# Performance work log

Hardware: AMD Instinct MI355X
Metric: run time of the kernel (lower is better)

## Reference

```python
import jax, jax.numpy as jnp
import numpy as np

B, N, F, C = 8, 4096, 1024, 64


def setup_inputs() -> dict:
    key = jax.random.key(0)
    k1, k2, k3 = jax.random.split(key, 3)
    x1 = jax.random.normal(k1, (B, N, F), dtype=jnp.float32)
    x2 = jax.random.normal(k2, (B, N, F), dtype=jnp.float32)
    W = jax.random.normal(k3, (C, F), dtype=jnp.float32) / np.sqrt(F)
    b = jnp.zeros((C,), dtype=jnp.float32)
    return {"x1": x1, "x2": x2, "W": W, "b": b}


def _select_max(x, W, b):
    # x: [B, N, F] -> scores [B, N, C]
    scores = jnp.einsum("bnf,cf->bnc", x, W) + b
    # per-batch, per-class index of max-scoring instance: [B, C]
    idx = jnp.argmax(scores, axis=1)
    # gather the selected instance feature vectors: [B, C, F]
    return jnp.take_along_axis(x, idx[:, :, None], axis=1)


def reference(x1, x2, W, b):
    d = _select_max(x1, W, b)
    d1 = _select_max(x2, W, b)
    return (d, d1)
```

## Files before the change

kernel.cpp:

```cpp
#include <hip/hip_runtime.h>

#define B_   8
#define N_   4096
#define F_   1024
#define C_   64
#define MARGIN 0.08f

typedef __attribute__((ext_vector_type(8))) short bhalf8;
typedef __attribute__((ext_vector_type(4))) float f32x4;

__device__ __forceinline__ unsigned short f2bf_rne(float x) {
    unsigned u = __builtin_bit_cast(unsigned, x);
    u += 0x7fffu + ((u >> 16) & 1u);
    return (unsigned short)(u >> 16);
}
__device__ __forceinline__ bhalf8 cvt8(float4 a, float4 b) {
    bhalf8 r;
    r[0] = (short)f2bf_rne(a.x); r[1] = (short)f2bf_rne(a.y);
    r[2] = (short)f2bf_rne(a.z); r[3] = (short)f2bf_rne(a.w);
    r[4] = (short)f2bf_rne(b.x); r[5] = (short)f2bf_rne(b.y);
    r[6] = (short)f2bf_rne(b.z); r[7] = (short)f2bf_rne(b.w);
    return r;
}

#define LEXGT(a, ai, b, bi) ((a) > (b) || ((a) == (b) && (ai) < (bi)))
#define INSERT3(vv, nn)                                                        \
    do {                                                                       \
        float _v = (vv); int _n = (nn);                                        \
        if (LEXGT(_v, _n, v0, i0)) { v2=v1; i2=i1; v1=v0; i1=i0; v0=_v; i0=_n; } \
        else if (LEXGT(_v, _n, v1, i1)) { v2=v1; i2=i1; v1=_v; i1=_n; }        \
        else if (LEXGT(_v, _n, v2, i2)) { v2=_v; i2=_n; }                      \
    } while (0)
#define INSERT4(vv, nn)                                                        \
    do {                                                                       \
        float _v = (vv); int _n = (nn);                                        \
        if (LEXGT(_v, _n, v0, i0)) { v3=v2; i3=i2; v2=v1; i2=i1; v1=v0; i1=i0; v0=_v; i0=_n; } \
        else if (LEXGT(_v, _n, v1, i1)) { v3=v2; i3=i2; v2=v1; i2=i1; v1=_v; i1=_n; } \
        else if (LEXGT(_v, _n, v2, i2)) { v3=v2; i3=i2; v2=_v; i2=_n; }        \
        else if (LEXGT(_v, _n, v3, i3)) { v3=_v; i3=_n; }                      \
    } while (0)

__global__ __launch_bounds__(512, 2) void score_top_kernel(
    const float* __restrict__ x1, const float* __restrict__ x2,
    const float* __restrict__ W,
    float* __restrict__ pv, int* __restrict__ pi)
{
    __shared__ __align__(16) char lds[131072];

    const int tid  = threadIdx.x;
    const int nb   = blockIdx.x;
    const int b    = blockIdx.y;
    const int inp  = blockIdx.z;
    const float* __restrict__ x = inp ? x2 : x1;

    const int lane = tid & 63;
    const int w    = tid >> 6;
    const int rsel = lane & 15;
    const int g    = lane >> 4;
    const int swz  = (rsel & 7) << 4;

    #pragma unroll
    for (int j = 0; j < 16; ++j) {
        int gi = tid + 512 * j;
        int c = gi >> 7, kq = gi & 127;
        const float* src = W + (size_t)c * F_ + kq * 8;
        float4 a  = *(const float4*)src;
        float4 bq = *(const float4*)(src + 4);
        int off = (c * 2048 + kq * 16) ^ ((c & 7) << 4);
        *(bhalf8*)(lds + off) = cvt8(a, bq);
    }

    const int row = nb * 128 + w * 16 + rsel;
    const float* __restrict__ xr = x + ((size_t)b * N_ + row) * F_ + g * 8;

    f32x4 acc[4];
    #pragma unroll
    for (int nt = 0; nt < 4; ++nt) acc[nt] = (f32x4){0.f, 0.f, 0.f, 0.f};

    auto loadx = [&](float4* dst, int kc) {
        #pragma unroll
        for (int st = 0; st < 2; ++st) {
            dst[2 * st]     = *(const float4*)(xr + kc * 64 + st * 32);
            dst[2 * st + 1] = *(const float4*)(xr + kc * 64 + st * 32 + 4);
        }
    };
    auto compute = [&](const float4* src, int kc) {
        #pragma unroll
        for (int st = 0; st < 2; ++st) {
            bhalf8 ah = cvt8(src[2 * st], src[2 * st + 1]);
            int kb = (kc * 64 + st * 32 + g * 8) * 2;
            #pragma unroll
            for (int nt = 0; nt < 4; ++nt) {
                int cls = nt * 16 + rsel;
                bhalf8 bf = *(const bhalf8*)(lds + ((cls * 2048 + kb) ^ swz));
                acc[nt] = __builtin_amdgcn_mfma_f32_16x16x32_bf16(ah, bf, acc[nt], 0, 0, 0);
            }
        }
    };

    float4 xa[4], xb[4];
    loadx(xa, 0);
    __syncthreads();

    #pragma unroll
    for (int kc = 0; kc < 16; kc += 2) {
        loadx(xb, kc + 1);
        compute(xa, kc);
        if (kc + 2 < 16) loadx(xa, kc + 2);
        compute(xb, kc + 1);
    }

    float wv0[4], wv1[4], wv2[4]; int wi0[4], wi1[4], wi2[4];
    #pragma unroll
    for (int nt = 0; nt < 4; ++nt) {
        float v0 = -3.4e38f, v1 = -3.4e38f, v2 = -3.4e38f;
        int   i0 = 0x7fffffff, i1 = 0x7fffffff, i2 = 0x7fffffff;
        #pragma unroll
        for (int r = 0; r < 4; ++r) {
            int n = nb * 128 + w * 16 + 4 * g + r;
            INSERT3(acc[nt][r], n);
        }
        #pragma unroll
        for (int d = 16; d <= 32; d <<= 1) {
            float u0 = __shfl_xor(v0, d), u1 = __shfl_xor(v1, d), u2 = __shfl_xor(v2, d);
            int   j0 = __shfl_xor(i0, d), j1 = __shfl_xor(i1, d), j2 = __shfl_xor(i2, d);
            INSERT3(u0, j0); INSERT3(u1, j1); INSERT3(u2, j2);
        }
        wv0[nt] = v0; wv1[nt] = v1; wv2[nt] = v2;
        wi0[nt] = i0; wi1[nt] = i1; wi2[nt] = i2;
    }

    __syncthreads();
    float* tv = (float*)lds;
    int*   ti = (int*)(lds + 6144);
    if (lane < 16) {
        #pragma unroll
        for (int nt = 0; nt < 4; ++nt) {
            int c = nt * 16 + lane;
            tv[(w * C_ + c) * 3 + 0] = wv0[nt]; ti[(w * C_ + c) * 3 + 0] = wi0[nt];
            tv[(w * C_ + c) * 3 + 1] = wv1[nt]; ti[(w * C_ + c) * 3 + 1] = wi1[nt];
            tv[(w * C_ + c) * 3 + 2] = wv2[nt]; ti[(w * C_ + c) * 3 + 2] = wi2[nt];
        }
    }
    __syncthreads();

    if (tid < C_) {
        int c = tid;
        float v0 = -3.4e38f, v1 = -3.4e38f, v2 = -3.4e38f, v3 = -3.4e38f;
        int   i0 = 0x7fffffff, i1 = 0x7fffffff, i2 = 0x7fffffff, i3 = 0x7fffffff;
        #pragma unroll
        for (int ww = 0; ww < 8; ++ww)
            #pragma unroll
            for (int k = 0; k < 3; ++k)
                INSERT4(tv[(ww * C_ + c) * 3 + k], ti[(ww * C_ + c) * 3 + k]);
        int blk = ((inp * B_ + b) * 32 + nb);
        pv[(blk * C_ + c) * 4 + 0] = v0; pi[(blk * C_ + c) * 4 + 0] = i0;
        pv[(blk * C_ + c) * 4 + 1] = v1; pi[(blk * C_ + c) * 4 + 1] = i1;
        pv[(blk * C_ + c) * 4 + 2] = v2; pi[(blk * C_ + c) * 4 + 2] = i2;
        pv[(blk * C_ + c) * 4 + 3] = v3; pi[(blk * C_ + c) * 4 + 3] = i3;
    }
}

__global__ __launch_bounds__(256) void select_gather_kernel(
    const float* __restrict__ x1, const float* __restrict__ x2,
    const float* __restrict__ W,
    const float* __restrict__ pv, const int* __restrict__ pi,
    float* __restrict__ out)
{
    const int c   = blockIdx.x;
    const int b   = blockIdx.y;
    const int inp = blockIdx.z;
    const int tid = threadIdx.x;

    __shared__ int   s_cnt;
    __shared__ float s_m[2];
    __shared__ int   s_cand[16];
    __shared__ float s_val[16];
    __shared__ float s_wsum[4];
    __shared__ int   s_win;

    if (tid == 0) s_cnt = 0;
    __syncthreads();

    float v = -3.4e38f;
    int myoff = 0;
    if (tid < 128) {
        int nb = tid >> 2, k = tid & 3;
        int blk = ((inp * B_ + b) * 32 + nb);
        myoff = (blk * C_ + c) * 4 + k;
        v = pv[myoff];
    }
    {
        float m = v;
        #pragma unroll
        for (int d = 32; d; d >>= 1) m = fmaxf(m, __shfl_xor(m, d));
        if ((tid & 63) == 0 && tid < 128) s_m[tid >> 6] = m;
    }
    __syncthreads();
    const float m = fmaxf(s_m[0], s_m[1]);
    if (tid < 128 && v >= m - MARGIN) {
        int p = atomicAdd(&s_cnt, 1);
        if (p < 16) s_cand[p] = pi[myoff];
    }
    __syncthreads();

    const float* __restrict__ x = inp ? x2 : x1;
    const int ncand = min(s_cnt, 16);
    int winner;
    if (ncand == 1) {
        winner = s_cand[0];
    } else {
        for (int k = 0; k < ncand; ++k) {
            int n = s_cand[k];
            float4 xv = *(const float4*)(x + ((size_t)b * N_ + n) * F_ + tid * 4);
            float4 wq = *(const float4*)(W + (size_t)c * F_ + tid * 4);
            float p = xv.x * wq.x + xv.y * wq.y + xv.z * wq.z + xv.w * wq.w;
            #pragma unroll
            for (int d = 32; d; d >>= 1) p += __shfl_down(p, d);
            if ((tid & 63) == 0) s_wsum[tid >> 6] = p;
            __syncthreads();
            if (tid == 0) s_val[k] = s_wsum[0] + s_wsum[1] + s_wsum[2] + s_wsum[3];
            __syncthreads();
        }
        if (tid == 0) {
            float bv = s_val[0]; int bn = s_cand[0];
            for (int k = 1; k < ncand; ++k)
                if (s_val[k] > bv || (s_val[k] == bv && s_cand[k] < bn)) { bv = s_val[k]; bn = s_cand[k]; }
            s_win = bn;
        }
        __syncthreads();
        winner = s_win;
    }

    float4 vv = *(const float4*)(x + ((size_t)b * N_ + winner) * F_ + tid * 4);
    *(float4*)(out + (((size_t)inp * B_ + b) * C_ + c) * F_ + tid * 4) = vv;
}

extern "C" void kernel_launch(void* const* d_in, const int* in_sizes, int n_in,
                              void* d_out, int out_size, void* d_ws, size_t ws_size,
                              hipStream_t stream) {
    const float* x1 = (const float*)d_in[0];
    const float* x2 = (const float*)d_in[1];
    const float* W  = (const float*)d_in[2];

    float* pv = (float*)d_ws;
    int*   pi = (int*)((char*)d_ws + (size_t)2 * B_ * 32 * C_ * 4 * sizeof(float));

    dim3 g1(32, B_, 2);
    score_top_kernel<<<g1, 512, 0, stream>>>(x1, x2, W, pv, pi);
    dim3 g2(C_, B_, 2);
    select_gather_kernel<<<g2, 256, 0, stream>>>(x1, x2, W, pv, pi, (float*)d_out);
}
```

Measured before the change: 78.25 us.

## Pre-convert W to bf16 and use 1024-thread blocks covering 256 rows

After: 72.49 us. 1.08x faster.

```diff
diff --git a/kernel.cpp b/kernel.cpp
--- a/kernel.cpp
+++ b/kernel.cpp
@@ -4,10 +4,12 @@
 #define N_   4096
 #define F_   1024
 #define C_   64
+#define NBLK 16
 #define MARGIN 0.08f
 
 typedef __attribute__((ext_vector_type(8))) short bhalf8;
 typedef __attribute__((ext_vector_type(4))) float f32x4;
+typedef __attribute__((ext_vector_type(4))) unsigned short us4;
 
 __device__ __forceinline__ unsigned short f2bf_rne(float x) {
     unsigned u = __builtin_bit_cast(unsigned, x);
@@ -40,9 +42,20 @@
         else if (LEXGT(_v, _n, v3, i3)) { v3=_v; i3=_n; }                      \
     } while (0)
 
-__global__ __launch_bounds__(512, 2) void score_top_kernel(
+__global__ __launch_bounds__(256) void wconv_kernel(
+    const float* __restrict__ W, unsigned short* __restrict__ Wh)
+{
+    int i = blockIdx.x * 256 + threadIdx.x;
+    float4 v = ((const float4*)W)[i];
+    us4 hh;
+    hh[0] = f2bf_rne(v.x); hh[1] = f2bf_rne(v.y);
+    hh[2] = f2bf_rne(v.z); hh[3] = f2bf_rne(v.w);
+    ((us4*)Wh)[i] = hh;
+}
+
+__global__ __launch_bounds__(1024, 4) void score_top_kernel(
     const float* __restrict__ x1, const float* __restrict__ x2,
-    const float* __restrict__ W,
+    const unsigned short* __restrict__ Wh,
     float* __restrict__ pv, int* __restrict__ pi)
 {
     __shared__ __align__(16) char lds[131072];
@@ -59,18 +72,7 @@
     const int g    = lane >> 4;
     const int swz  = (rsel & 7) << 4;
 
-    #pragma unroll
-    for (int j = 0; j < 16; ++j) {
-        int gi = tid + 512 * j;
-        int c = gi >> 7, kq = gi & 127;
-        const float* src = W + (size_t)c * F_ + kq * 8;
-        float4 a  = *(const float4*)src;
-        float4 bq = *(const float4*)(src + 4);
-        int off = (c * 2048 + kq * 16) ^ ((c & 7) << 4);
-        *(bhalf8*)(lds + off) = cvt8(a, bq);
-    }
-
-    const int row = nb * 128 + w * 16 + rsel;
+    const int row = nb * 256 + w * 16 + rsel;
     const float* __restrict__ xr = x + ((size_t)b * N_ + row) * F_ + g * 8;
 
     f32x4 acc[4];
@@ -79,16 +81,16 @@
 
     auto loadx = [&](float4* dst, int kc) {
         #pragma unroll
-        for (int st = 0; st < 2; ++st) {
-            dst[2 * st]     = *(const float4*)(xr + kc * 64 + st * 32);
-            dst[2 * st + 1] = *(const float4*)(xr + kc * 64 + st * 32 + 4);
+        for (int st = 0; st < 4; ++st) {
+            dst[2 * st]     = *(const float4*)(xr + kc * 128 + st * 32);
+            dst[2 * st + 1] = *(const float4*)(xr + kc * 128 + st * 32 + 4);
         }
     };
     auto compute = [&](const float4* src, int kc) {
         #pragma unroll
-        for (int st = 0; st < 2; ++st) {
+        for (int st = 0; st < 4; ++st) {
             bhalf8 ah = cvt8(src[2 * st], src[2 * st + 1]);
-            int kb = (kc * 64 + st * 32 + g * 8) * 2;
+            int kb = kc * 256 + st * 64 + g * 16;
             #pragma unroll
             for (int nt = 0; nt < 4; ++nt) {
                 int cls = nt * 16 + rsel;
@@ -98,15 +100,23 @@
         }
     };
 
-    float4 xa[4], xb[4];
+    float4 xa[8], xb[8];
     loadx(xa, 0);
-    __syncthreads();
-
-    #pragma unroll
-    for (int kc = 0; kc < 16; kc += 2) {
+
+    #pragma unroll
+    for (int j = 0; j < 8; ++j) {
+        int gi = tid + 1024 * j;
+        int c = gi >> 7, kq = gi & 127;
+        bhalf8 v = *(const bhalf8*)(Wh + (size_t)c * F_ + kq * 8);
+        *(bhalf8*)(lds + ((c * 2048 + kq * 16) ^ ((c & 7) << 4))) = v;
+    }
+    __syncthreads();
+
+    #pragma unroll
+    for (int kc = 0; kc < 8; kc += 2) {
         loadx(xb, kc + 1);
         compute(xa, kc);
-        if (kc + 2 < 16) loadx(xa, kc + 2);
+        if (kc + 2 < 8) loadx(xa, kc + 2);
         compute(xb, kc + 1);
     }
 
@@ -117,7 +127,7 @@
         int   i0 = 0x7fffffff, i1 = 0x7fffffff, i2 = 0x7fffffff;
         #pragma unroll
         for (int r = 0; r < 4; ++r) {
-            int n = nb * 128 + w * 16 + 4 * g + r;
+            int n = nb * 256 + w * 16 + 4 * g + r;
             INSERT3(acc[nt][r], n);
         }
         #pragma unroll
@@ -132,7 +142,7 @@
 
     __syncthreads();
     float* tv = (float*)lds;
-    int*   ti = (int*)(lds + 6144);
+    int*   ti = (int*)(lds + 16384);
     if (lane < 16) {
         #pragma unroll
         for (int nt = 0; nt < 4; ++nt) {
@@ -148,12 +158,12 @@
         int c = tid;
         float v0 = -3.4e38f, v1 = -3.4e38f, v2 = -3.4e38f, v3 = -3.4e38f;
         int   i0 = 0x7fffffff, i1 = 0x7fffffff, i2 = 0x7fffffff, i3 = 0x7fffffff;
-        #pragma unroll
-        for (int ww = 0; ww < 8; ++ww)
+        #pragma unroll 4
+        for (int ww = 0; ww < 16; ++ww)
             #pragma unroll
             for (int k = 0; k < 3; ++k)
                 INSERT4(tv[(ww * C_ + c) * 3 + k], ti[(ww * C_ + c) * 3 + k]);
-        int blk = ((inp * B_ + b) * 32 + nb);
+        int blk = ((inp * B_ + b) * NBLK + nb);
         pv[(blk * C_ + c) * 4 + 0] = v0; pi[(blk * C_ + c) * 4 + 0] = i0;
         pv[(blk * C_ + c) * 4 + 1] = v1; pi[(blk * C_ + c) * 4 + 1] = i1;
         pv[(blk * C_ + c) * 4 + 2] = v2; pi[(blk * C_ + c) * 4 + 2] = i2;
@@ -173,7 +183,7 @@
     const int tid = threadIdx.x;
 
     __shared__ int   s_cnt;
-    __shared__ float s_m[2];
+    __shared__ float s_m;
     __shared__ int   s_cand[16];
     __shared__ float s_val[16];
     __shared__ float s_wsum[4];
@@ -182,25 +192,19 @@
     if (tid == 0) s_cnt = 0;
     __syncthreads();
 
-    float v = -3.4e38f;
-    int myoff = 0;
-    if (tid < 128) {
+    if (tid < 64) {
         int nb = tid >> 2, k = tid & 3;
-        int blk = ((inp * B_ + b) * 32 + nb);
-        myoff = (blk * C_ + c) * 4 + k;
-        v = pv[myoff];
-    }
-    {
+        int blk = ((inp * B_ + b) * NBLK + nb);
+        int myoff = (blk * C_ + c) * 4 + k;
+        float v = pv[myoff];
         float m = v;
         #pragma unroll
         for (int d = 32; d; d >>= 1) m = fmaxf(m, __shfl_xor(m, d));
-        if ((tid & 63) == 0 && tid < 128) s_m[tid >> 6] = m;
-    }
-    __syncthreads();
-    const float m = fmaxf(s_m[0], s_m[1]);
-    if (tid < 128 && v >= m - MARGIN) {
-        int p = atomicAdd(&s_cnt, 1);
-        if (p < 16) s_cand[p] = pi[myoff];
+        if (tid == 0) s_m = m;
+        if (v >= m - MARGIN) {
+            int p = atomicAdd(&s_cnt, 1);
+            if (p < 16) s_cand[p] = pi[myoff];
+        }
     }
     __syncthreads();
 
@@ -243,11 +247,13 @@
     const float* x2 = (const float*)d_in[1];
     const float* W  = (const float*)d_in[2];
 
-    float* pv = (float*)d_ws;
-    int*   pi = (int*)((char*)d_ws + (size_t)2 * B_ * 32 * C_ * 4 * sizeof(float));
-
-    dim3 g1(32, B_, 2);
-    score_top_kernel<<<g1, 512, 0, stream>>>(x1, x2, W, pv, pi);
+    unsigned short* Wh = (unsigned short*)d_ws;
+    float* pv = (float*)((char*)d_ws + (size_t)C_ * F_ * sizeof(unsigned short));
+    int*   pi = (int*)((char*)pv + (size_t)2 * B_ * NBLK * C_ * 4 * sizeof(float));
+
+    wconv_kernel<<<C_ * F_ / 1024, 256, 0, stream>>>(W, Wh);
+    dim3 g1(NBLK, B_, 2);
+    score_top_kernel<<<g1, 1024, 0, stream>>>(x1, x2, Wh, pv, pi);
     dim3 g2(C_, B_, 2);
     select_gather_kernel<<<g2, 256, 0, stream>>>(x1, x2, W, pv, pi, (float*)d_out);
 }
```
